# Kernel tuning notes

Hardware: AMD Instinct MI355X
Metric: run time of the kernel (lower is better)

## Reference

```python
import jax, jax.numpy as jnp
import numpy as np

N_EMBD = 384
NUM_HEADS = 6


def setup_inputs() -> dict:
    key = jax.random.key(0)
    k1, k2, k3 = jax.random.split(key, 3)
    b, t = 128, 256
    X = jax.random.normal(k1, (b, t, N_EMBD), dtype=jnp.float32)
    Wqkv = jax.random.normal(k2, (N_EMBD, 3 * N_EMBD), dtype=jnp.float32) * 0.02
    Wproj = jax.random.normal(k3, (N_EMBD, N_EMBD), dtype=jnp.float32) * 0.02
    return {"X": X, "Wqkv": Wqkv, "Wproj": Wproj}


def reference(X, Wqkv, Wproj):
    b, t, c = X.shape
    d = c // NUM_HEADS
    # fused QKV projection; split order in the source is K, Q, V
    qkv = X @ Wqkv  # (b, t, 3c)
    K, Q, V = jnp.split(qkv, 3, axis=-1)
    # (b, t, H, d) -> (b, H, t, d)
    K = K.reshape(b, t, NUM_HEADS, d).transpose(0, 2, 1, 3)
    Q = Q.reshape(b, t, NUM_HEADS, d).transpose(0, 2, 1, 3)
    V = V.reshape(b, t, NUM_HEADS, d).transpose(0, 2, 1, 3)
    # NOTE: faithful quirk — scale by full embed dim c, not head_size
    scale = c ** (-0.5)
    W = jnp.einsum("bhqd,bhkd->bhqk", Q, K) * scale  # (b, H, t, t)
    causal = jnp.tril(jnp.ones((t, t), dtype=bool))
    W = jnp.where(causal, W, -jnp.inf)
    W = jax.nn.softmax(W, axis=-1)
    # dropout layers are identity in eval mode
    OUT = jnp.einsum("bhqk,bhkd->bhqd", W, V)  # (b, H, t, d)
    OUT = OUT.transpose(0, 2, 1, 3).reshape(b, t, c)
    return OUT @ Wproj
```

## Files before the change

### kernel.cpp

```cpp
#include <hip/hip_runtime.h>
#include <hip/hip_bf16.h>

#define BATCH 128
#define TSEQ  256
#define NEMBD 384
#define NHEAD 6
#define HDIM  64
#define C3    1152
#define MROWS 32768
#define KGTOT 48
#define NBH   768
#define BHSZ  16384

typedef __attribute__((ext_vector_type(8))) short short8v;
typedef __attribute__((ext_vector_type(4))) float float4v;


__device__ __forceinline__ float bf2f(unsigned short u) {
  union { unsigned int i; float f; } x;
  x.i = ((unsigned int)u) << 16;
  return x.f;
}

__device__ __forceinline__ unsigned short f2bf(float f) {
  __hip_bfloat16 h = __float2bfloat16(f);
  unsigned short u;
  __builtin_memcpy(&u, &h, 2);
  return u;
}

__global__ __launch_bounds__(256)
void convertA(const float* __restrict__ X, unsigned short* __restrict__ out) {
  const int idx = blockIdx.x * 256 + threadIdx.x;
  const int ml  = idx & 127;
  const int kgg = (idx >> 7) % KGTOT;
  const int mb  = idx / (128 * KGTOT);
  const float* src = X + ((size_t)(mb * 128 + ml) * NEMBD + kgg * 8);
  float4 a = *reinterpret_cast<const float4*>(src);
  float4 b = *reinterpret_cast<const float4*>(src + 4);
  short8v v;
  v[0] = (short)f2bf(a.x); v[1] = (short)f2bf(a.y);
  v[2] = (short)f2bf(a.z); v[3] = (short)f2bf(a.w);
  v[4] = (short)f2bf(b.x); v[5] = (short)f2bf(b.y);
  v[6] = (short)f2bf(b.z); v[7] = (short)f2bf(b.w);
  *reinterpret_cast<short8v*>(out + (size_t)idx * 8) = v;
}

__global__ __launch_bounds__(256)
void convertB(const float* __restrict__ W, unsigned short* __restrict__ out, int N) {
  const int idx = blockIdx.x * 256 + threadIdx.x;
  const int nl  = idx & 127;
  const int kgg = (idx >> 7) % KGTOT;
  const int nb  = idx / (128 * KGTOT);
  const int n = nb * 128 + nl;
  short8v v;
#pragma unroll
  for (int j = 0; j < 8; ++j)
    v[j] = (short)f2bf(W[(size_t)(kgg * 8 + j) * N + n]);
  *reinterpret_cast<short8v*>(out + (size_t)idx * 8) = v;
}


#define GEMM_CORE(Ab, Bb)                                                              \
  __shared__ __attribute__((aligned(16))) unsigned short Asl[4096];                    \
  __shared__ __attribute__((aligned(16))) unsigned short Bsl[4096];                    \
  const int tid  = threadIdx.x;                                                        \
  const int wave = tid >> 6;                                                           \
  const int lane = tid & 63;                                                           \
  const int wm  = (wave & 1) * 64;                                                     \
  const int wn  = (wave >> 1) * 64;                                                    \
  const int l15 = lane & 15;                                                           \
  const int lq  = lane >> 4;                                                           \
  float4v acc[4][4];                                                                   \
  _Pragma("unroll") for (int i = 0; i < 4; ++i)                                        \
    _Pragma("unroll") for (int j = 0; j < 4; ++j)                                      \
      acc[i][j] = (float4v){0.f, 0.f, 0.f, 0.f};                                       \
  const int ldsb0 = wave * 64 * 8;                                                     \
  for (int kb = 0; kb < KGTOT / 4; ++kb) {                                             \
    __syncthreads();                                                                   \
    _Pragma("unroll") for (int r = 0; r < 2; ++r) {                                    \
      const int i = r * 256 + tid;                                                     \
      const size_t goff = ((size_t)(kb * 4 + (i >> 7)) * 128 + (i & 127)) * 8;         \
      const int lb = ldsb0 + r * 2048;                                                 \
      __builtin_amdgcn_global_load_lds(                                                \
          (const __attribute__((address_space(1))) unsigned int*)(Ab + goff),          \
          (__attribute__((address_space(3))) unsigned int*)(Asl + lb), 16, 0, 0);      \
      __builtin_amdgcn_global_load_lds(                                                \
          (const __attribute__((address_space(1))) unsigned int*)(Bb + goff),          \
          (__attribute__((address_space(3))) unsigned int*)(Bsl + lb), 16, 0, 0);      \
    }                                                                                  \
    __syncthreads();                                                                   \
    short8v af[4], bfr[4];                                                             \
    _Pragma("unroll") for (int mi = 0; mi < 4; ++mi)                                   \
      af[mi] = *reinterpret_cast<const short8v*>(                                      \
          Asl + (size_t)(lq * 128 + wm + mi * 16 + l15) * 8);                          \
    _Pragma("unroll") for (int ni = 0; ni < 4; ++ni)                                   \
      bfr[ni] = *reinterpret_cast<const short8v*>(                                     \
          Bsl + (size_t)(lq * 128 + wn + ni * 16 + l15) * 8);                          \
    _Pragma("unroll") for (int mi = 0; mi < 4; ++mi)                                   \
      _Pragma("unroll") for (int ni = 0; ni < 4; ++ni)                                 \
        acc[mi][ni] = __builtin_amdgcn_mfma_f32_16x16x32_bf16(af[mi], bfr[ni],         \
                                                              acc[mi][ni], 0, 0, 0);   \
  }

__global__ __launch_bounds__(256)
void gemm_qkv(const unsigned short* __restrict__ A,
              const unsigned short* __restrict__ B,
              unsigned short* __restrict__ KQV) {
  const int ord   = blockIdx.x;
  const int xcd   = ord & 7;
  const int g     = ord >> 3;
  const int mtile = xcd * 32 + (g & 31);
  const int ntile = g >> 5;
  const unsigned short* Ab = A + (size_t)mtile * (KGTOT * 128 * 8);
  const unsigned short* Bb = B + (size_t)ntile * (KGTOT * 128 * 8);
  GEMM_CORE(Ab, Bb)
  const int colb = ntile * 128 + wn + l15;
  const int rowb = mtile * 128 + wm + lq * 4;
  if (ntile >= 6) {
    unsigned short* Vb = KQV + (size_t)(2 * NBH) * BHSZ;
#pragma unroll
    for (int ni = 0; ni < 4; ++ni) {
      const int rem = colb + ni * 16 - 768;
      const int hh  = rem >> 6;
      const int d   = rem & 63;
#pragma unroll
      for (int mi = 0; mi < 4; ++mi) {
        const int m  = rowb + mi * 16;
        const int bb = m >> 8;
        const int tt = m & 255;
        ushort4 v;
        v.x = f2bf(acc[mi][ni][0]); v.y = f2bf(acc[mi][ni][1]);
        v.z = f2bf(acc[mi][ni][2]); v.w = f2bf(acc[mi][ni][3]);
        *reinterpret_cast<ushort4*>(
            Vb + (size_t)(bb * NHEAD + hh) * BHSZ + (tt >> 3) * 512 + d * 8 + (tt & 7)) = v;
      }
    }
  } else {
    const int type = (ntile >= 3) ? 1 : 0;
    const float sc = type ? 0.051031036307982884f : 1.0f;
    unsigned short* outb = KQV + (size_t)type * NBH * BHSZ;
#pragma unroll
    for (int ni = 0; ni < 4; ++ni) {
      const int rem = colb + ni * 16 - type * 384;
      const int hh  = rem >> 6;
      const int d   = rem & 63;
      const int dg  = d >> 3;
      const int dl  = d & 7;
#pragma unroll
      for (int mi = 0; mi < 4; ++mi) {
#pragma unroll
        for (int r = 0; r < 4; ++r) {
          const int m  = rowb + mi * 16 + r;
          const int bb = m >> 8;
          const int tt = m & 255;
          outb[(size_t)(bb * NHEAD + hh) * BHSZ + dg * 2048 + tt * 8 + dl] =
              f2bf(acc[mi][ni][r] * sc);
        }
      }
    }
  }
}

__global__ __launch_bounds__(256)
void gemm_proj(const unsigned short* __restrict__ A,
               const unsigned short* __restrict__ B,
               float* __restrict__ C, int N) {
  const int ord   = blockIdx.x;
  const int xcd   = ord & 7;
  const int g     = ord >> 3;
  const int mtile = xcd * 32 + (g & 31);
  const int ntile = g >> 5;
  const unsigned short* Ab = A + (size_t)mtile * (KGTOT * 128 * 8);
  const unsigned short* Bb = B + (size_t)ntile * (KGTOT * 128 * 8);
  GEMM_CORE(Ab, Bb)
  const int colbase = ntile * 128 + wn + l15;
  const int rowbase = mtile * 128 + wm + lq * 4;
#pragma unroll
  for (int mi = 0; mi < 4; ++mi)
#pragma unroll
    for (int ni = 0; ni < 4; ++ni)
#pragma unroll
      for (int r = 0; r < 4; ++r)
        C[(size_t)(rowbase + mi * 16 + r) * N + colbase + ni * 16] = acc[mi][ni][r];
}

__global__ __launch_bounds__(256, 3)
void attn_mfma(const unsigned short* __restrict__ KQV,
               unsigned short* __restrict__ Obf) {
  const int bh   = blockIdx.x;
  const int b    = bh / NHEAD;
  const int h    = bh - b * NHEAD;
  const int tid  = threadIdx.x;
  const int wave = tid >> 6;
  const int lane = tid & 63;
  const int l15  = lane & 15;
  const int lq   = lane >> 4;

  __shared__ __attribute__((aligned(16))) unsigned short Kls[16384];
  __shared__ __attribute__((aligned(16))) unsigned short Pt[4][1024];

  const unsigned short* Kb = KQV + (size_t)bh * BHSZ;
  const unsigned short* Qb = KQV + (size_t)(NBH + bh) * BHSZ;
  const unsigned short* Vb = KQV + (size_t)(2 * NBH + bh) * BHSZ;

#pragma unroll
  for (int r = 0; r < 8; ++r) {
    const int i = r * 256 + tid;
    __builtin_amdgcn_global_load_lds(
        (const __attribute__((address_space(1))) unsigned int*)(Kb + (size_t)i * 8),
        (__attribute__((address_space(3))) unsigned int*)(Kls + i * 8), 16, 0, 0);
  }
  __syncthreads();

  unsigned short* Pw = Pt[wave];

  for (int j = 0; j < 4; ++j) {
    short8v qa[2];
#pragma unroll
    for (int s = 0; s < 2; ++s)
      qa[s] = *reinterpret_cast<const short8v*>(
          Qb + (size_t)(s * 4 + lq) * 2048 + (size_t)(j * 64 + wave * 16 + l15) * 8);

    float4v o[4];
#pragma unroll
    for (int nf = 0; nf < 4; ++nf) o[nf] = (float4v){0.f, 0.f, 0.f, 0.f};
    float4v lp = (float4v){0.f, 0.f, 0.f, 0.f};

    for (int kt = 0; kt <= j; ++kt) {
      short8v vf[2][4];
#pragma unroll
      for (int s = 0; s < 2; ++s)
#pragma unroll
        for (int nf = 0; nf < 4; ++nf)
          vf[s][nf] = *reinterpret_cast<const short8v*>(
              Vb + (size_t)(kt * 8 + s * 4 + lq) * 512 + (size_t)(nf * 16 + l15) * 8);

      float4v sf[4];
#pragma unroll
      for (int nf = 0; nf < 4; ++nf) sf[nf] = (float4v){0.f, 0.f, 0.f, 0.f};
#pragma unroll
      for (int s = 0; s < 2; ++s) {
        short8v kf[4];
#pragma unroll
        for (int nf = 0; nf < 4; ++nf)
          kf[nf] = *reinterpret_cast<const short8v*>(
              Kls + (size_t)(s * 4 + lq) * 2048 + (size_t)(kt * 64 + nf * 16 + l15) * 8);
#pragma unroll
        for (int nf = 0; nf < 4; ++nf)
          sf[nf] = __builtin_amdgcn_mfma_f32_16x16x32_bf16(qa[s], kf[nf], sf[nf], 0, 0, 0);
      }

      if (kt == j) {
        const int qit = wave * 16 + lq * 4;
#pragma unroll
        for (int nf = 0; nf < 4; ++nf) {
          const int key = nf * 16 + l15;
#pragma unroll
          for (int r = 0; r < 4; ++r)
            if (key > qit + r) sf[nf][r] = -INFINITY;
        }
      }

#pragma unroll
      for (int nf = 0; nf < 4; ++nf) {
        const int kg  = nf * 2 + (l15 >> 3);
        const int pos = l15 & 7;
#pragma unroll
        for (int r = 0; r < 4; ++r) {
          const float p = __expf(sf[nf][r]);
          lp[r] += p;
          Pw[(kg * 16 + lq * 4 + r) * 8 + pos] = f2bf(p);
        }
      }

#pragma unroll
      for (int s = 0; s < 2; ++s) {
        short8v pa = *reinterpret_cast<const short8v*>(
            Pw + (size_t)((s * 4 + lq) * 16 + l15) * 8);
#pragma unroll
        for (int nf = 0; nf < 4; ++nf)
          o[nf] = __builtin_amdgcn_mfma_f32_16x16x32_bf16(pa, vf[s][nf], o[nf], 0, 0, 0);
      }
    }

#pragma unroll
    for (int off = 1; off <= 8; off <<= 1)
#pragma unroll
      for (int r = 0; r < 4; ++r)
        lp[r] += __shfl_xor(lp[r], off);
    float4v inv;
#pragma unroll
    for (int r = 0; r < 4; ++r) inv[r] = 1.f / lp[r];

    const int tq = j * 64 + wave * 16 + lq * 4;
#pragma unroll
    for (int nf = 0; nf < 4; ++nf) {
      const int d   = nf * 16 + l15;
      const int gg  = h * 8 + (d >> 3);
      const int pos = d & 7;
#pragma unroll
      for (int r = 0; r < 4; ++r) {
        const int m = b * TSEQ + tq + r;
        Obf[((size_t)(m >> 7) * KGTOT + gg) * 1024 + (size_t)(m & 127) * 8 + pos] =
            f2bf(o[nf][r] * inv[r]);
      }
    }
  }
}


extern "C" void kernel_launch(void* const* d_in, const int* in_sizes, int n_in,
                              void* d_out, int out_size, void* d_ws, size_t ws_size,
                              hipStream_t stream) {
  const float* X     = (const float*)d_in[0];
  const float* Wqkv  = (const float*)d_in[1];
  const float* Wproj = (const float*)d_in[2];
  float* out = (float*)d_out;

  unsigned short* KQV    = (unsigned short*)d_ws;
  unsigned short* Abf    = (unsigned short*)((char*)d_ws + 75497472);
  unsigned short* WqkvT  = (unsigned short*)((char*)d_ws + 75497472 + 25165824);
  unsigned short* WprojT = (unsigned short*)((char*)d_ws + 75497472 + 25165824 + 884736);
  unsigned short* Obf    = Abf;

  dim3 blk(256);
  convertA<<<dim3((MROWS * KGTOT) / 256), blk, 0, stream>>>(X, Abf);
  convertB<<<dim3((C3 * KGTOT) / 256), blk, 0, stream>>>(Wqkv, WqkvT, C3);
  convertB<<<dim3((NEMBD * KGTOT) / 256), blk, 0, stream>>>(Wproj, WprojT, NEMBD);

  gemm_qkv<<<dim3(2304), blk, 0, stream>>>(Abf, WqkvT, KQV);
  attn_mfma<<<dim3(NBH), blk, 0, stream>>>(KQV, Obf);
  gemm_proj<<<dim3(768), blk, 0, stream>>>(Obf, WprojT, out, NEMBD);
}
```

Baseline: 196.4 us.

## Stage QKV epilogue through LDS, double K-tile depth, merge conversion kernels

The QKV GEMM epilogue now writes the accumulators into shared memory (padded layouts, in two halves) and then issues coalesced 16-byte stores into the per-head K/Q/V layouts. This replaces the scattered 2-byte and 8-byte global stores. The GEMM core now loads 8 k-groups per barrier pair instead of 4, which halves the number of syncs but doubles the LDS footprint to 32KB. The three fp32-to-bf16 conversion kernels are merged into one launch to cut launch overhead.

```diff
diff --git a/kernel.cpp b/kernel.cpp
--- a/kernel.cpp
+++ b/kernel.cpp
@@ -12,6 +12,10 @@
 #define NBH   768
 #define BHSZ  16384
 
+#define NA_CH  (MROWS * KGTOT)
+#define NW1_CH (C3 * KGTOT)
+#define NW2_CH (NEMBD * KGTOT)
+
 typedef __attribute__((ext_vector_type(8))) short short8v;
 typedef __attribute__((ext_vector_type(4))) float float4v;
 
@@ -29,26 +33,13 @@
   return u;
 }
 
-__global__ __launch_bounds__(256)
-void convertA(const float* __restrict__ X, unsigned short* __restrict__ out) {
-  const int idx = blockIdx.x * 256 + threadIdx.x;
-  const int ml  = idx & 127;
-  const int kgg = (idx >> 7) % KGTOT;
-  const int mb  = idx / (128 * KGTOT);
-  const float* src = X + ((size_t)(mb * 128 + ml) * NEMBD + kgg * 8);
-  float4 a = *reinterpret_cast<const float4*>(src);
-  float4 b = *reinterpret_cast<const float4*>(src + 4);
-  short8v v;
-  v[0] = (short)f2bf(a.x); v[1] = (short)f2bf(a.y);
-  v[2] = (short)f2bf(a.z); v[3] = (short)f2bf(a.w);
-  v[4] = (short)f2bf(b.x); v[5] = (short)f2bf(b.y);
-  v[6] = (short)f2bf(b.z); v[7] = (short)f2bf(b.w);
-  *reinterpret_cast<short8v*>(out + (size_t)idx * 8) = v;
-}
-
-__global__ __launch_bounds__(256)
-void convertB(const float* __restrict__ W, unsigned short* __restrict__ out, int N) {
-  const int idx = blockIdx.x * 256 + threadIdx.x;
+__device__ __forceinline__ unsigned int pack2bf(float a, float b) {
+  return (unsigned int)f2bf(a) | ((unsigned int)f2bf(b) << 16);
+}
+
+__device__ __forceinline__ void convB_body(const float* __restrict__ W,
+                                           unsigned short* __restrict__ out,
+                                           int N, int idx) {
   const int nl  = idx & 127;
   const int kgg = (idx >> 7) % KGTOT;
   const int nb  = idx / (128 * KGTOT);
@@ -60,10 +51,33 @@
   *reinterpret_cast<short8v*>(out + (size_t)idx * 8) = v;
 }
 
-
-#define GEMM_CORE(Ab, Bb)                                                              \
-  __shared__ __attribute__((aligned(16))) unsigned short Asl[4096];                    \
-  __shared__ __attribute__((aligned(16))) unsigned short Bsl[4096];                    \
+__global__ __launch_bounds__(256)
+void convert_all(const float* __restrict__ X, const float* __restrict__ W1,
+                 const float* __restrict__ W2, unsigned short* __restrict__ Abf,
+                 unsigned short* __restrict__ W1T, unsigned short* __restrict__ W2T) {
+  int idx = blockIdx.x * 256 + threadIdx.x;
+  if (idx < NA_CH) {
+    const int ml  = idx & 127;
+    const int kgg = (idx >> 7) % KGTOT;
+    const int mb  = idx / (128 * KGTOT);
+    const float* src = X + ((size_t)(mb * 128 + ml) * NEMBD + kgg * 8);
+    float4 a = *reinterpret_cast<const float4*>(src);
+    float4 b = *reinterpret_cast<const float4*>(src + 4);
+    short8v v;
+    v[0] = (short)f2bf(a.x); v[1] = (short)f2bf(a.y);
+    v[2] = (short)f2bf(a.z); v[3] = (short)f2bf(a.w);
+    v[4] = (short)f2bf(b.x); v[5] = (short)f2bf(b.y);
+    v[6] = (short)f2bf(b.z); v[7] = (short)f2bf(b.w);
+    *reinterpret_cast<short8v*>(Abf + (size_t)idx * 8) = v;
+  } else if (idx < NA_CH + NW1_CH) {
+    convB_body(W1, W1T, C3, idx - NA_CH);
+  } else {
+    convB_body(W2, W2T, NEMBD, idx - NA_CH - NW1_CH);
+  }
+}
+
+
+#define GEMM_CORE(Ab, Bb, ASL, BSL)                                                    \
   const int tid  = threadIdx.x;                                                        \
   const int wave = tid >> 6;                                                           \
   const int lane = tid & 63;                                                           \
@@ -75,38 +89,42 @@
   _Pragma("unroll") for (int i = 0; i < 4; ++i)                                        \
     _Pragma("unroll") for (int j = 0; j < 4; ++j)                                      \
       acc[i][j] = (float4v){0.f, 0.f, 0.f, 0.f};                                       \
-  const int ldsb0 = wave * 64 * 8;                                                     \
-  for (int kb = 0; kb < KGTOT / 4; ++kb) {                                             \
+  for (int kb = 0; kb < KGTOT / 8; ++kb) {                                             \
     __syncthreads();                                                                   \
-    _Pragma("unroll") for (int r = 0; r < 2; ++r) {                                    \
+    _Pragma("unroll") for (int r = 0; r < 4; ++r) {                                    \
       const int i = r * 256 + tid;                                                     \
-      const size_t goff = ((size_t)(kb * 4 + (i >> 7)) * 128 + (i & 127)) * 8;         \
-      const int lb = ldsb0 + r * 2048;                                                 \
+      const size_t goff = ((size_t)(kb * 8 + (i >> 7)) * 128 + (i & 127)) * 8;         \
       __builtin_amdgcn_global_load_lds(                                                \
           (const __attribute__((address_space(1))) unsigned int*)(Ab + goff),          \
-          (__attribute__((address_space(3))) unsigned int*)(Asl + lb), 16, 0, 0);      \
+          (__attribute__((address_space(3))) unsigned int*)(ASL + i * 8), 16, 0, 0);   \
       __builtin_amdgcn_global_load_lds(                                                \
           (const __attribute__((address_space(1))) unsigned int*)(Bb + goff),          \
-          (__attribute__((address_space(3))) unsigned int*)(Bsl + lb), 16, 0, 0);      \
+          (__attribute__((address_space(3))) unsigned int*)(BSL + i * 8), 16, 0, 0);   \
     }                                                                                  \
     __syncthreads();                                                                   \
-    short8v af[4], bfr[4];                                                             \
-    _Pragma("unroll") for (int mi = 0; mi < 4; ++mi)                                   \
-      af[mi] = *reinterpret_cast<const short8v*>(                                      \
-          Asl + (size_t)(lq * 128 + wm + mi * 16 + l15) * 8);                          \
-    _Pragma("unroll") for (int ni = 0; ni < 4; ++ni)                                   \
-      bfr[ni] = *reinterpret_cast<const short8v*>(                                     \
-          Bsl + (size_t)(lq * 128 + wn + ni * 16 + l15) * 8);                          \
-    _Pragma("unroll") for (int mi = 0; mi < 4; ++mi)                                   \
+    _Pragma("unroll") for (int s = 0; s < 2; ++s) {                                    \
+      short8v af[4], bfr[4];                                                           \
+      _Pragma("unroll") for (int mi = 0; mi < 4; ++mi)                                 \
+        af[mi] = *reinterpret_cast<const short8v*>(                                    \
+            ASL + (size_t)((s * 4 + lq) * 128 + wm + mi * 16 + l15) * 8);              \
       _Pragma("unroll") for (int ni = 0; ni < 4; ++ni)                                 \
-        acc[mi][ni] = __builtin_amdgcn_mfma_f32_16x16x32_bf16(af[mi], bfr[ni],         \
-                                                              acc[mi][ni], 0, 0, 0);   \
+        bfr[ni] = *reinterpret_cast<const short8v*>(                                   \
+            BSL + (size_t)((s * 4 + lq) * 128 + wn + ni * 16 + l15) * 8);              \
+      _Pragma("unroll") for (int mi = 0; mi < 4; ++mi)                                 \
+        _Pragma("unroll") for (int ni = 0; ni < 4; ++ni)                               \
+          acc[mi][ni] = __builtin_amdgcn_mfma_f32_16x16x32_bf16(af[mi], bfr[ni],       \
+                                                                acc[mi][ni], 0, 0, 0); \
+  }                                                                                    \
   }
 
 __global__ __launch_bounds__(256)
 void gemm_qkv(const unsigned short* __restrict__ A,
               const unsigned short* __restrict__ B,
               unsigned short* __restrict__ KQV) {
+  __shared__ __attribute__((aligned(16))) unsigned short S[16384];
+  unsigned short* ASL = S;
+  unsigned short* BSL = S + 8192;
+
   const int ord   = blockIdx.x;
   const int xcd   = ord & 7;
   const int g     = ord >> 3;
@@ -114,49 +132,78 @@
   const int ntile = g >> 5;
   const unsigned short* Ab = A + (size_t)mtile * (KGTOT * 128 * 8);
   const unsigned short* Bb = B + (size_t)ntile * (KGTOT * 128 * 8);
-  GEMM_CORE(Ab, Bb)
-  const int colb = ntile * 128 + wn + l15;
-  const int rowb = mtile * 128 + wm + lq * 4;
-  if (ntile >= 6) {
-    unsigned short* Vb = KQV + (size_t)(2 * NBH) * BHSZ;
-#pragma unroll
-    for (int ni = 0; ni < 4; ++ni) {
-      const int rem = colb + ni * 16 - 768;
-      const int hh  = rem >> 6;
-      const int d   = rem & 63;
-#pragma unroll
-      for (int mi = 0; mi < 4; ++mi) {
-        const int m  = rowb + mi * 16;
-        const int bb = m >> 8;
-        const int tt = m & 255;
-        ushort4 v;
-        v.x = f2bf(acc[mi][ni][0]); v.y = f2bf(acc[mi][ni][1]);
-        v.z = f2bf(acc[mi][ni][2]); v.w = f2bf(acc[mi][ni][3]);
-        *reinterpret_cast<ushort4*>(
-            Vb + (size_t)(bb * NHEAD + hh) * BHSZ + (tt >> 3) * 512 + d * 8 + (tt & 7)) = v;
+  GEMM_CORE(Ab, Bb, ASL, BSL)
+
+  const int type = (ntile >= 6) ? 2 : (ntile >= 3 ? 1 : 0);
+  const int rel  = ntile - type * 3;
+  const int hh0  = rel * 2;
+  const float sc = (type == 1) ? 0.051031036307982884f : 1.0f;
+  unsigned short* outb = KQV + (size_t)type * NBH * BHSZ;
+  unsigned int* Ct32 = reinterpret_cast<unsigned int*>(S);
+
+#pragma unroll
+  for (int p = 0; p < 2; ++p) {
+    __syncthreads();
+    if ((wave & 1) == p) {
+      if (type < 2) {
+#pragma unroll
+        for (int mi = 0; mi < 4; ++mi)
+#pragma unroll
+          for (int ni = 0; ni < 4; ++ni) {
+            const int col = wn + ni * 16 + l15;
+#pragma unroll
+            for (int r = 0; r < 4; ++r)
+              S[(mi * 16 + lq * 4 + r) * 130 + col] = f2bf(acc[mi][ni][r] * sc);
+          }
+      } else {
+#pragma unroll
+        for (int mi = 0; mi < 4; ++mi)
+#pragma unroll
+          for (int ni = 0; ni < 4; ++ni) {
+            const int col  = wn + ni * 16 + l15;
+            const int base = col * 33 + mi * 8 + lq * 2;
+            Ct32[base]     = pack2bf(acc[mi][ni][0], acc[mi][ni][1]);
+            Ct32[base + 1] = pack2bf(acc[mi][ni][2], acc[mi][ni][3]);
+          }
       }
     }
-  } else {
-    const int type = (ntile >= 3) ? 1 : 0;
-    const float sc = type ? 0.051031036307982884f : 1.0f;
-    unsigned short* outb = KQV + (size_t)type * NBH * BHSZ;
-#pragma unroll
-    for (int ni = 0; ni < 4; ++ni) {
-      const int rem = colb + ni * 16 - type * 384;
-      const int hh  = rem >> 6;
-      const int d   = rem & 63;
-      const int dg  = d >> 3;
-      const int dl  = d & 7;
-#pragma unroll
-      for (int mi = 0; mi < 4; ++mi) {
-#pragma unroll
-        for (int r = 0; r < 4; ++r) {
-          const int m  = rowb + mi * 16 + r;
-          const int bb = m >> 8;
-          const int tt = m & 255;
-          outb[(size_t)(bb * NHEAD + hh) * BHSZ + dg * 2048 + tt * 8 + dl] =
-              f2bf(acc[mi][ni][r] * sc);
-        }
+    __syncthreads();
+    const int m0p = mtile * 128 + p * 64;
+    const int bb  = m0p >> 8;
+    const int tt0 = m0p & 255;
+    if (type < 2) {
+      const int mloc = tid & 63;
+      const int w4   = tid >> 6;
+#pragma unroll
+      for (int it = 0; it < 4; ++it) {
+        const int hdgl = w4 * 4 + it;
+        const int hh   = hh0 + (hdgl >> 3);
+        const int dg   = hdgl & 7;
+        uint4 v;
+        v.x = Ct32[mloc * 65 + hdgl * 4 + 0];
+        v.y = Ct32[mloc * 65 + hdgl * 4 + 1];
+        v.z = Ct32[mloc * 65 + hdgl * 4 + 2];
+        v.w = Ct32[mloc * 65 + hdgl * 4 + 3];
+        *reinterpret_cast<uint4*>(
+            outb + (size_t)(bb * NHEAD + hh) * BHSZ + dg * 2048 +
+            (size_t)(tt0 + mloc) * 8) = v;
+      }
+    } else {
+      const int colloc = tid & 127;
+      const int half   = tid >> 7;
+      const int hh = hh0 + (colloc >> 6);
+      const int d  = colloc & 63;
+#pragma unroll
+      for (int it = 0; it < 4; ++it) {
+        const int tgl = half * 4 + it;
+        uint4 v;
+        v.x = Ct32[colloc * 33 + tgl * 4 + 0];
+        v.y = Ct32[colloc * 33 + tgl * 4 + 1];
+        v.z = Ct32[colloc * 33 + tgl * 4 + 2];
+        v.w = Ct32[colloc * 33 + tgl * 4 + 3];
+        *reinterpret_cast<uint4*>(
+            outb + (size_t)(bb * NHEAD + hh) * BHSZ +
+            (size_t)((tt0 >> 3) + tgl) * 512 + d * 8) = v;
       }
     }
   }
@@ -166,6 +213,10 @@
 void gemm_proj(const unsigned short* __restrict__ A,
                const unsigned short* __restrict__ B,
                float* __restrict__ C, int N) {
+  __shared__ __attribute__((aligned(16))) unsigned short S[16384];
+  unsigned short* ASL = S;
+  unsigned short* BSL = S + 8192;
+
   const int ord   = blockIdx.x;
   const int xcd   = ord & 7;
   const int g     = ord >> 3;
@@ -173,7 +224,7 @@
   const int ntile = g >> 5;
   const unsigned short* Ab = A + (size_t)mtile * (KGTOT * 128 * 8);
   const unsigned short* Bb = B + (size_t)ntile * (KGTOT * 128 * 8);
-  GEMM_CORE(Ab, Bb)
+  GEMM_CORE(Ab, Bb, ASL, BSL)
   const int colbase = ntile * 128 + wn + l15;
   const int rowbase = mtile * 128 + wm + lq * 4;
 #pragma unroll
@@ -325,10 +376,8 @@
   unsigned short* Obf    = Abf;
 
   dim3 blk(256);
-  convertA<<<dim3((MROWS * KGTOT) / 256), blk, 0, stream>>>(X, Abf);
-  convertB<<<dim3((C3 * KGTOT) / 256), blk, 0, stream>>>(Wqkv, WqkvT, C3);
-  convertB<<<dim3((NEMBD * KGTOT) / 256), blk, 0, stream>>>(Wproj, WprojT, NEMBD);
-
+  convert_all<<<dim3((NA_CH + NW1_CH + NW2_CH) / 256), blk, 0, stream>>>(
+      X, Wqkv, Wproj, Abf, WqkvT, WprojT);
   gemm_qkv<<<dim3(2304), blk, 0, stream>>>(Abf, WqkvT, KQV);
   attn_mfma<<<dim3(NBH), blk, 0, stream>>>(KQV, Obf);
   gemm_proj<<<dim3(768), blk, 0, stream>>>(Obf, WprojT, out, NEMBD);
```

Result: no change. 199.9 us (+1.8%).

## Double-buffer GEMM LDS staging and merge conversion kernels into one launch

Applied to the files above, without the earlier changes.

The shared GEMM core now uses two LDS buffers. It prefetches the next K block with global_load_lds while MFMAs run on the current block, which also drops one barrier per iteration. The three fp32-to-bf16 conversion kernels are folded into a single launch that dispatches on the thread index. LDS use per block doubles to 32KB. Overlap depends on the compiler not placing a full vmcnt wait before the LDS reads.

```diff
diff --git a/kernel.cpp b/kernel.cpp
--- a/kernel.cpp
+++ b/kernel.cpp
@@ -12,6 +12,10 @@
 #define NBH   768
 #define BHSZ  16384
 
+#define NA_CH  (MROWS * KGTOT)
+#define NW1_CH (C3 * KGTOT)
+#define NW2_CH (NEMBD * KGTOT)
+
 typedef __attribute__((ext_vector_type(8))) short short8v;
 typedef __attribute__((ext_vector_type(4))) float float4v;
 
@@ -29,26 +33,9 @@
   return u;
 }
 
-__global__ __launch_bounds__(256)
-void convertA(const float* __restrict__ X, unsigned short* __restrict__ out) {
-  const int idx = blockIdx.x * 256 + threadIdx.x;
-  const int ml  = idx & 127;
-  const int kgg = (idx >> 7) % KGTOT;
-  const int mb  = idx / (128 * KGTOT);
-  const float* src = X + ((size_t)(mb * 128 + ml) * NEMBD + kgg * 8);
-  float4 a = *reinterpret_cast<const float4*>(src);
-  float4 b = *reinterpret_cast<const float4*>(src + 4);
-  short8v v;
-  v[0] = (short)f2bf(a.x); v[1] = (short)f2bf(a.y);
-  v[2] = (short)f2bf(a.z); v[3] = (short)f2bf(a.w);
-  v[4] = (short)f2bf(b.x); v[5] = (short)f2bf(b.y);
-  v[6] = (short)f2bf(b.z); v[7] = (short)f2bf(b.w);
-  *reinterpret_cast<short8v*>(out + (size_t)idx * 8) = v;
-}
-
-__global__ __launch_bounds__(256)
-void convertB(const float* __restrict__ W, unsigned short* __restrict__ out, int N) {
-  const int idx = blockIdx.x * 256 + threadIdx.x;
+__device__ __forceinline__ void convB_body(const float* __restrict__ W,
+                                           unsigned short* __restrict__ out,
+                                           int N, int idx) {
   const int nl  = idx & 127;
   const int kgg = (idx >> 7) % KGTOT;
   const int nb  = idx / (128 * KGTOT);
@@ -60,10 +47,46 @@
   *reinterpret_cast<short8v*>(out + (size_t)idx * 8) = v;
 }
 
+__global__ __launch_bounds__(256)
+void convert_all(const float* __restrict__ X, const float* __restrict__ W1,
+                 const float* __restrict__ W2, unsigned short* __restrict__ Abf,
+                 unsigned short* __restrict__ W1T, unsigned short* __restrict__ W2T) {
+  int idx = blockIdx.x * 256 + threadIdx.x;
+  if (idx < NA_CH) {
+    const int ml  = idx & 127;
+    const int kgg = (idx >> 7) % KGTOT;
+    const int mb  = idx / (128 * KGTOT);
+    const float* src = X + ((size_t)(mb * 128 + ml) * NEMBD + kgg * 8);
+    float4 a = *reinterpret_cast<const float4*>(src);
+    float4 b = *reinterpret_cast<const float4*>(src + 4);
+    short8v v;
+    v[0] = (short)f2bf(a.x); v[1] = (short)f2bf(a.y);
+    v[2] = (short)f2bf(a.z); v[3] = (short)f2bf(a.w);
+    v[4] = (short)f2bf(b.x); v[5] = (short)f2bf(b.y);
+    v[6] = (short)f2bf(b.z); v[7] = (short)f2bf(b.w);
+    *reinterpret_cast<short8v*>(Abf + (size_t)idx * 8) = v;
+  } else if (idx < NA_CH + NW1_CH) {
+    convB_body(W1, W1T, C3, idx - NA_CH);
+  } else {
+    convB_body(W2, W2T, NEMBD, idx - NA_CH - NW1_CH);
+  }
+}
+
+
+#define GEMM_STAGE(Ab, Bb, kb, ASL, BSL)                                               \
+  _Pragma("unroll") for (int r = 0; r < 2; ++r) {                                      \
+    const int i = r * 256 + tid;                                                       \
+    const size_t goff = ((size_t)((kb) * 4 + (i >> 7)) * 128 + (i & 127)) * 8;         \
+    __builtin_amdgcn_global_load_lds(                                                  \
+        (const __attribute__((address_space(1))) unsigned int*)((Ab) + goff),          \
+        (__attribute__((address_space(3))) unsigned int*)((ASL) + i * 8), 16, 0, 0);   \
+    __builtin_amdgcn_global_load_lds(                                                  \
+        (const __attribute__((address_space(1))) unsigned int*)((Bb) + goff),          \
+        (__attribute__((address_space(3))) unsigned int*)((BSL) + i * 8), 16, 0, 0);   \
+  }
 
 #define GEMM_CORE(Ab, Bb)                                                              \
-  __shared__ __attribute__((aligned(16))) unsigned short Asl[4096];                    \
-  __shared__ __attribute__((aligned(16))) unsigned short Bsl[4096];                    \
+  __shared__ __attribute__((aligned(16))) unsigned short S[16384];                     \
   const int tid  = threadIdx.x;                                                        \
   const int wave = tid >> 6;                                                           \
   const int lane = tid & 63;                                                           \
@@ -75,28 +98,21 @@
   _Pragma("unroll") for (int i = 0; i < 4; ++i)                                        \
     _Pragma("unroll") for (int j = 0; j < 4; ++j)                                      \
       acc[i][j] = (float4v){0.f, 0.f, 0.f, 0.f};                                       \
-  const int ldsb0 = wave * 64 * 8;                                                     \
+  GEMM_STAGE(Ab, Bb, 0, S, S + 4096)                                                   \
   for (int kb = 0; kb < KGTOT / 4; ++kb) {                                             \
+    const int cur = (kb & 1) * 8192;                                                   \
+    const int nxt = 8192 - cur;                                                        \
     __syncthreads();                                                                   \
-    _Pragma("unroll") for (int r = 0; r < 2; ++r) {                                    \
-      const int i = r * 256 + tid;                                                     \
-      const size_t goff = ((size_t)(kb * 4 + (i >> 7)) * 128 + (i & 127)) * 8;         \
-      const int lb = ldsb0 + r * 2048;                                                 \
-      __builtin_amdgcn_global_load_lds(                                                \
-          (const __attribute__((address_space(1))) unsigned int*)(Ab + goff),          \
-          (__attribute__((address_space(3))) unsigned int*)(Asl + lb), 16, 0, 0);      \
-      __builtin_amdgcn_global_load_lds(                                                \
-          (const __attribute__((address_space(1))) unsigned int*)(Bb + goff),          \
-          (__attribute__((address_space(3))) unsigned int*)(Bsl + lb), 16, 0, 0);      \
+    if (kb + 1 < KGTOT / 4) {                                                          \
+      GEMM_STAGE(Ab, Bb, kb + 1, S + nxt, S + nxt + 4096)                              \
     }                                                                                  \
-    __syncthreads();                                                                   \
     short8v af[4], bfr[4];                                                             \
     _Pragma("unroll") for (int mi = 0; mi < 4; ++mi)                                   \
       af[mi] = *reinterpret_cast<const short8v*>(                                      \
-          Asl + (size_t)(lq * 128 + wm + mi * 16 + l15) * 8);                          \
+          S + cur + (size_t)(lq * 128 + wm + mi * 16 + l15) * 8);                      \
     _Pragma("unroll") for (int ni = 0; ni < 4; ++ni)                                   \
       bfr[ni] = *reinterpret_cast<const short8v*>(                                     \
-          Bsl + (size_t)(lq * 128 + wn + ni * 16 + l15) * 8);                          \
+          S + cur + 4096 + (size_t)(lq * 128 + wn + ni * 16 + l15) * 8);               \
     _Pragma("unroll") for (int mi = 0; mi < 4; ++mi)                                   \
       _Pragma("unroll") for (int ni = 0; ni < 4; ++ni)                                 \
         acc[mi][ni] = __builtin_amdgcn_mfma_f32_16x16x32_bf16(af[mi], bfr[ni],         \
@@ -325,10 +341,8 @@
   unsigned short* Obf    = Abf;
 
   dim3 blk(256);
-  convertA<<<dim3((MROWS * KGTOT) / 256), blk, 0, stream>>>(X, Abf);
-  convertB<<<dim3((C3 * KGTOT) / 256), blk, 0, stream>>>(Wqkv, WqkvT, C3);
-  convertB<<<dim3((NEMBD * KGTOT) / 256), blk, 0, stream>>>(Wproj, WprojT, NEMBD);
-
+  convert_all<<<dim3((NA_CH + NW1_CH + NW2_CH) / 256), blk, 0, stream>>>(
+      X, Wqkv, Wproj, Abf, WqkvT, WprojT);
   gemm_qkv<<<dim3(2304), blk, 0, stream>>>(Abf, WqkvT, KQV);
   attn_mfma<<<dim3(NBH), blk, 0, stream>>>(KQV, Obf);
   gemm_proj<<<dim3(768), blk, 0, stream>>>(Obf, WprojT, out, NEMBD);
```

Result: faster. 186.6 us (-5.0%).
